# Kernel optimization log

Hardware: AMD Instinct MI355X
Metric: run time of the kernel (lower is better)

## Reference

```python
import jax, jax.numpy as jnp
import numpy as np


def setup_inputs() -> dict:
    key = jax.random.key(0)
    k1, k2, k3, k4 = jax.random.split(key, 4)
    B, C_in, C_out, E, K = 4, 128, 256, 30000, 5
    x = jax.random.normal(k1, (B, C_in, E, 1), dtype=jnp.float32)
    ne_idx = jax.random.randint(k2, (B, E, K - 1), 0, E, dtype=jnp.int32)
    conv_w = jax.random.normal(k3, (C_out, C_in, 1, K), dtype=jnp.float32) * 0.05
    conv_b = jax.random.normal(k4, (C_out,), dtype=jnp.float32) * 0.05
    return {"x": x, "ne_idx": ne_idx, "conv_w": conv_w, "conv_b": conv_b}


def reference(x, ne_idx, conv_w, conv_b):
    # x: [B, C, E, 1] edge features; ne_idx: [B, E, 4] neighbor edge ids.
    B, C, E, _ = x.shape
    xs = x[..., 0]                                        # [B, C, E]

    # pad_graph_mat: prepend self index column -> [B, E, 5]
    self_idx = jnp.broadcast_to(
        jnp.arange(E, dtype=ne_idx.dtype)[None, :, None], (B, E, 1))
    idx = jnp.concatenate([self_idx, ne_idx], axis=2) + 1  # +1 for zero pad slot

    # zero-pad feature dim so index 0 maps to zeros (matches torch padding col)
    x_pad = jnp.pad(xs, ((0, 0), (0, 0), (1, 0)))          # [B, C, E+1]

    # gather: f[b, c, e, k] = x_pad[b, c, idx[b, e, k]]
    f = jax.vmap(lambda xp, i: xp[:, i])(x_pad, idx)       # [B, C, E, 5]

    e0, e1, e2, e3, e4 = (f[..., j] for j in range(5))
    p = e1 + e3
    q = e2 + e4
    p1 = jnp.abs(e1 - e3)
    q1 = jnp.abs(e2 - e4)
    G = jnp.stack([e0, p, q, p1, q1], axis=-1)             # [B, C, E, 5]

    # Conv2d with kernel (1, 5): contraction over in-channels and the 5 taps
    out = jnp.einsum('bcek,ocuk->boe', G, conv_w) + conv_b[None, :, None]
    return out[..., None]                                  # [B, C_out, E, 1]
```

## Files before the change

### kernel.cpp

```cpp
#include <hip/hip_runtime.h>
#include <hip/hip_bf16.h>
#include <stdint.h>

#define E_N   30000
#define C_IN  128
#define C_OUT 256
#define B_N   4
#define KTAP  5
#define BN    64
#define KSTEPS 20

typedef short bf16x8 __attribute__((ext_vector_type(8)));
typedef float f32x4  __attribute__((ext_vector_type(4)));

static __device__ __forceinline__ unsigned short f2bf(float f) {
    union { float f; uint32_t u; } v; v.f = f;
    uint32_t r = (v.u + 0x7FFFu + ((v.u >> 16) & 1u)) >> 16;
    return (unsigned short)r;
}
static __device__ __forceinline__ float bf2f(uint32_t h) {
    union { uint32_t u; float f; } v; v.u = h << 16;
    return v.f;
}

__global__ void pack_w_kernel(const float* __restrict__ w,
                              unsigned short* __restrict__ wp) {
    int tid = blockIdx.x * blockDim.x + threadIdx.x;
    if (tid >= KSTEPS * 16 * 64) return;
    int s    = tid >> 10;
    int mt   = (tid >> 6) & 15;
    int lane = tid & 63;
    int m    = mt * 16 + (lane & 15);
    int kb   = s * 32 + ((lane >> 4) & 3) * 8;
    uint32_t pv[4];
    for (int jj = 0; jj < 4; ++jj) {
        unsigned short lo, hi;
        {
            int kk = kb + 2 * jj;
            int t = kk >> 7, c = kk & 127;
            lo = f2bf(w[(m * C_IN + c) * KTAP + t]);
        }
        {
            int kk = kb + 2 * jj + 1;
            int t = kk >> 7, c = kk & 127;
            hi = f2bf(w[(m * C_IN + c) * KTAP + t]);
        }
        pv[jj] = (uint32_t)lo | ((uint32_t)hi << 16);
    }
    uint4 val; val.x = pv[0]; val.y = pv[1]; val.z = pv[2]; val.w = pv[3];
    *(uint4*)(wp + (size_t)tid * 8) = val;
}

__global__ void transpose_kernel(const float* __restrict__ x,
                                 unsigned short* __restrict__ xT) {
    __shared__ float ld[C_IN][64 + 1];
    int b  = blockIdx.y;
    int e0 = blockIdx.x * 64;
    int t  = threadIdx.x;
    bool full = (e0 + 64 <= E_N);
    for (int pass = 0; pass < 8; ++pass) {
        int c  = pass * 16 + (t >> 4);
        int eo = (t & 15) * 4;
        if (full) {
            const float4 v = *(const float4*)(x + ((size_t)(b * C_IN + c) * E_N + e0 + eo));
            ld[c][eo] = v.x; ld[c][eo + 1] = v.y; ld[c][eo + 2] = v.z; ld[c][eo + 3] = v.w;
        } else {
            for (int i = 0; i < 4; ++i) {
                int e = e0 + eo + i;
                ld[c][eo + i] = (e < E_N) ? x[(size_t)(b * C_IN + c) * E_N + e] : 0.f;
            }
        }
    }
    __syncthreads();
    for (int pass = 0; pass < 8; ++pass) {
        int el = pass * 8 + (t >> 5);
        int c0 = (t & 31) * 4;
        int e  = e0 + el;
        if (e < E_N) {
            ushort4 v;
            v.x = f2bf(ld[c0 + 0][el]);
            v.y = f2bf(ld[c0 + 1][el]);
            v.z = f2bf(ld[c0 + 2][el]);
            v.w = f2bf(ld[c0 + 3][el]);
            *(ushort4*)(xT + (size_t)(b * E_N + e) * C_IN + c0) = v;
        }
    }
}

__launch_bounds__(256)
__global__ void mesh_gemm(const unsigned short* __restrict__ wp,
                          const unsigned short* __restrict__ xT,
                          const int* __restrict__ ne,
                          const float* __restrict__ bias,
                          float* __restrict__ out) {
    __shared__ __align__(16) unsigned short gbuf[BN][40];
    __shared__ int nbr[BN][4];

    int b    = blockIdx.y;
    int e0   = blockIdx.x * BN;
    int tid  = threadIdx.x;
    int lane = tid & 63;
    int wave = tid >> 6;

    {
        int col = tid >> 2, j = tid & 3;
        int e = e0 + col; if (e >= E_N) e = E_N - 1;
        nbr[col][j] = ne[((size_t)b * E_N + e) * 4 + j];
    }
    __syncthreads();

    f32x4 acc[4][4];
    for (int mt = 0; mt < 4; ++mt)
        for (int nt = 0; nt < 4; ++nt)
            acc[mt][nt] = (f32x4){0.f, 0.f, 0.f, 0.f};

    const int col    = tid >> 2;
    const int c8     = (tid & 3) * 8;
    int self_e       = e0 + col; if (self_e >= E_N) self_e = E_N - 1;
    const uint4* wp16 = (const uint4*)wp;

    for (int s = 0; s < KSTEPS; ++s) {
        const int tap = s >> 2;
        const int cb  = (s & 3) * 32;

        bf16x8 af[4];
        for (int mt = 0; mt < 4; ++mt) {
            int mtg = wave * 4 + mt;
            uint4 v = wp16[(s * 16 + mtg) * 64 + lane];
            af[mt] = *(bf16x8*)&v;
        }

        __syncthreads();

        {
            uint4 gval;
            if (tap == 0) {
                gval = *(const uint4*)(xT + ((size_t)(b * E_N + self_e) * C_IN + cb + c8));
            } else {
                int j1 = (tap == 1 || tap == 3) ? 0 : 1;
                int s1 = nbr[col][j1];
                int s2 = nbr[col][j1 + 2];
                uint4 v1 = *(const uint4*)(xT + ((size_t)(b * E_N + s1) * C_IN + cb + c8));
                uint4 v2 = *(const uint4*)(xT + ((size_t)(b * E_N + s2) * C_IN + cb + c8));
                const bool isabs = (tap >= 3);
                uint32_t* a1 = (uint32_t*)&v1;
                uint32_t* a2 = (uint32_t*)&v2;
                uint32_t* g  = (uint32_t*)&gval;
                for (int i = 0; i < 4; ++i) {
                    float x0 = bf2f(a1[i] & 0xFFFFu), x1 = bf2f(a1[i] >> 16);
                    float y0 = bf2f(a2[i] & 0xFFFFu), y1 = bf2f(a2[i] >> 16);
                    float r0 = isabs ? fabsf(x0 - y0) : (x0 + y0);
                    float r1 = isabs ? fabsf(x1 - y1) : (x1 + y1);
                    g[i] = (uint32_t)f2bf(r0) | ((uint32_t)f2bf(r1) << 16);
                }
            }
            *(uint4*)(&gbuf[col][c8]) = gval;
        }
        __syncthreads();

        bf16x8 bfr[4];
        const int nl_lo = lane & 15;
        const int k8    = ((lane >> 4) & 3) * 8;
        for (int nt = 0; nt < 4; ++nt)
            bfr[nt] = *(const bf16x8*)(&gbuf[nt * 16 + nl_lo][k8]);

        for (int nt = 0; nt < 4; ++nt)
            for (int mt = 0; mt < 4; ++mt)
                acc[mt][nt] = __builtin_amdgcn_mfma_f32_16x16x32_bf16(
                    af[mt], bfr[nt], acc[mt][nt], 0, 0, 0);
    }

    const int quad = lane >> 4;
    const int ecol = lane & 15;
    for (int mt = 0; mt < 4; ++mt) {
        int o_base = (wave * 4 + mt) * 16 + quad * 4;
        for (int r = 0; r < 4; ++r) {
            int o = o_base + r;
            float bv = bias[o];
            for (int nt = 0; nt < 4; ++nt) {
                int e = e0 + nt * 16 + ecol;
                if (e < E_N)
                    out[((size_t)(b * C_OUT + o)) * E_N + e] = acc[mt][nt][r] + bv;
            }
        }
    }
}

__global__ void fallback_kernel(const float* __restrict__ x,
                                const int* __restrict__ ne,
                                const float* __restrict__ w,
                                const float* __restrict__ bias,
                                float* __restrict__ out) {
    size_t id = (size_t)blockIdx.x * blockDim.x + threadIdx.x;
    if (id >= (size_t)B_N * C_OUT * E_N) return;
    int e = (int)(id % E_N);
    int o = (int)((id / E_N) % C_OUT);
    int b = (int)(id / ((size_t)E_N * C_OUT));
    const int4 nb = *(const int4*)(ne + ((size_t)b * E_N + e) * 4);
    float acc = bias[o];
    for (int c = 0; c < C_IN; ++c) {
        const float* xb = x + (size_t)(b * C_IN + c) * E_N;
        float s0 = xb[e];
        float x1 = xb[nb.x], x2 = xb[nb.y], x3 = xb[nb.z], x4 = xb[nb.w];
        const float* wo = w + (size_t)(o * C_IN + c) * KTAP;
        acc += wo[0] * s0
             + wo[1] * (x1 + x3)
             + wo[2] * (x2 + x4)
             + wo[3] * fabsf(x1 - x3)
             + wo[4] * fabsf(x2 - x4);
    }
    out[id] = acc;
}

extern "C" void kernel_launch(void* const* d_in, const int* in_sizes, int n_in,
                              void* d_out, int out_size, void* d_ws, size_t ws_size,
                              hipStream_t stream) {
    const float* x      = (const float*)d_in[0];
    const int*   ne_idx = (const int*)d_in[1];
    const float* conv_w = (const float*)d_in[2];
    const float* conv_b = (const float*)d_in[3];
    float* out = (float*)d_out;

    const size_t wp_bytes = (size_t)C_OUT * 640 * 2;
    const size_t xT_off   = 512 * 1024;
    const size_t need     = xT_off + (size_t)B_N * E_N * C_IN * 2;

    if (ws_size < need) {
        size_t total = (size_t)B_N * C_OUT * E_N;
        int blocks = (int)((total + 255) / 256);
        fallback_kernel<<<blocks, 256, 0, stream>>>(x, ne_idx, conv_w, conv_b, out);
        return;
    }
    (void)wp_bytes;

    unsigned short* wp = (unsigned short*)d_ws;
    unsigned short* xT = (unsigned short*)((char*)d_ws + xT_off);

    pack_w_kernel<<<80, 256, 0, stream>>>(conv_w, wp);
    dim3 tg((E_N + 63) / 64, B_N);
    transpose_kernel<<<tg, 256, 0, stream>>>(x, xT);
    dim3 gg((E_N + BN - 1) / BN, B_N);
    mesh_gemm<<<gg, 256, 0, stream>>>(wp, xT, ne_idx, conv_b, out);
}
```

Measured before the change: 256.3 us.

## Restructure mesh GEMM to gather all taps per channel chunk with prefetch

The main loop now runs over channel chunks instead of tap-major k-steps. For each chunk it loads the self and four neighbor rows once, computes all five tap features into a five-slot shared buffer, and prefetches the next chunk's rows while the MFMAs for the current chunk run. This cuts the number of barriers from 40 to 8 and removes redundant neighbor reloads. It also widens the transpose stores to 16 bytes and makes the output stores nontemporal. In exchange it uses more LDS and registers, which may lower occupancy.

```diff
diff --git a/kernel.cpp b/kernel.cpp
--- a/kernel.cpp
+++ b/kernel.cpp
@@ -8,7 +8,6 @@
 #define B_N   4
 #define KTAP  5
 #define BN    64
-#define KSTEPS 20
 
 typedef short bf16x8 __attribute__((ext_vector_type(8)));
 typedef float f32x4  __attribute__((ext_vector_type(4)));
@@ -26,7 +25,7 @@
 __global__ void pack_w_kernel(const float* __restrict__ w,
                               unsigned short* __restrict__ wp) {
     int tid = blockIdx.x * blockDim.x + threadIdx.x;
-    if (tid >= KSTEPS * 16 * 64) return;
+    if (tid >= 20 * 16 * 64) return;
     int s    = tid >> 10;
     int mt   = (tid >> 6) & 15;
     int lane = tid & 63;
@@ -72,17 +71,19 @@
         }
     }
     __syncthreads();
-    for (int pass = 0; pass < 8; ++pass) {
-        int el = pass * 8 + (t >> 5);
-        int c0 = (t & 31) * 4;
+    for (int pass = 0; pass < 4; ++pass) {
+        int el = pass * 16 + (t >> 4);
+        int c0 = (t & 15) * 8;
         int e  = e0 + el;
         if (e < E_N) {
-            ushort4 v;
-            v.x = f2bf(ld[c0 + 0][el]);
-            v.y = f2bf(ld[c0 + 1][el]);
-            v.z = f2bf(ld[c0 + 2][el]);
-            v.w = f2bf(ld[c0 + 3][el]);
-            *(ushort4*)(xT + (size_t)(b * E_N + e) * C_IN + c0) = v;
+            uint32_t pk[4];
+            for (int i = 0; i < 4; ++i) {
+                unsigned short lo = f2bf(ld[c0 + 2 * i][el]);
+                unsigned short hi = f2bf(ld[c0 + 2 * i + 1][el]);
+                pk[i] = (uint32_t)lo | ((uint32_t)hi << 16);
+            }
+            uint4 v; v.x = pk[0]; v.y = pk[1]; v.z = pk[2]; v.w = pk[3];
+            *(uint4*)(xT + (size_t)(b * E_N + e) * C_IN + c0) = v;
         }
     }
 }
@@ -93,14 +94,14 @@
                           const int* __restrict__ ne,
                           const float* __restrict__ bias,
                           float* __restrict__ out) {
-    __shared__ __align__(16) unsigned short gbuf[BN][40];
+    __shared__ __align__(16) unsigned short gbuf[KTAP][BN][40];
     __shared__ int nbr[BN][4];
 
-    int b    = blockIdx.y;
-    int e0   = blockIdx.x * BN;
-    int tid  = threadIdx.x;
-    int lane = tid & 63;
-    int wave = tid >> 6;
+    const int b    = blockIdx.y;
+    const int e0   = blockIdx.x * BN;
+    const int tid  = threadIdx.x;
+    const int lane = tid & 63;
+    const int wave = tid >> 6;
 
     {
         int col = tid >> 2, j = tid & 3;
@@ -109,78 +110,113 @@
     }
     __syncthreads();
 
+    const int col = tid >> 2;
+    const int c8  = (tid & 3) * 8;
+    int self_e = e0 + col; if (self_e >= E_N) self_e = E_N - 1;
+    const int s1 = nbr[col][0], s2 = nbr[col][2];
+    const int s3 = nbr[col][1], s4 = nbr[col][3];
+
+    const unsigned short* xb = xT + (size_t)b * E_N * C_IN + c8;
+    const uint4* p0 = (const uint4*)(xb + (size_t)self_e * C_IN);
+    const uint4* p1 = (const uint4*)(xb + (size_t)s1 * C_IN);
+    const uint4* p2 = (const uint4*)(xb + (size_t)s2 * C_IN);
+    const uint4* p3 = (const uint4*)(xb + (size_t)s3 * C_IN);
+    const uint4* p4 = (const uint4*)(xb + (size_t)s4 * C_IN);
+
     f32x4 acc[4][4];
+#pragma unroll
     for (int mt = 0; mt < 4; ++mt)
+#pragma unroll
         for (int nt = 0; nt < 4; ++nt)
             acc[mt][nt] = (f32x4){0.f, 0.f, 0.f, 0.f};
 
-    const int col    = tid >> 2;
-    const int c8     = (tid & 3) * 8;
-    int self_e       = e0 + col; if (self_e >= E_N) self_e = E_N - 1;
     const uint4* wp16 = (const uint4*)wp;
-
-    for (int s = 0; s < KSTEPS; ++s) {
-        const int tap = s >> 2;
-        const int cb  = (s & 3) * 32;
-
-        bf16x8 af[4];
-        for (int mt = 0; mt < 4; ++mt) {
-            int mtg = wave * 4 + mt;
-            uint4 v = wp16[(s * 16 + mtg) * 64 + lane];
-            af[mt] = *(bf16x8*)&v;
-        }
+    const int nl = lane & 15;
+    const int k8 = (lane >> 4) * 8;
+
+    uint4 v0 = p0[0], v1 = p1[0], v2 = p2[0], v3 = p3[0], v4 = p4[0];
+
+#pragma unroll
+    for (int cbi = 0; cbi < 4; ++cbi) {
+        uint4 g1, g2, g3, g4;
+        {
+            const uint32_t* a = (const uint32_t*)&v1;
+            const uint32_t* c = (const uint32_t*)&v2;
+            uint32_t* o1 = (uint32_t*)&g1;
+            uint32_t* o3 = (uint32_t*)&g3;
+#pragma unroll
+            for (int i = 0; i < 4; ++i) {
+                float x0 = bf2f(a[i] & 0xFFFFu), x1 = bf2f(a[i] >> 16);
+                float y0 = bf2f(c[i] & 0xFFFFu), y1 = bf2f(c[i] >> 16);
+                o1[i] = (uint32_t)f2bf(x0 + y0) | ((uint32_t)f2bf(x1 + y1) << 16);
+                o3[i] = (uint32_t)f2bf(fabsf(x0 - y0)) | ((uint32_t)f2bf(fabsf(x1 - y1)) << 16);
+            }
+            const uint32_t* d = (const uint32_t*)&v3;
+            const uint32_t* e = (const uint32_t*)&v4;
+            uint32_t* o2 = (uint32_t*)&g2;
+            uint32_t* o4 = (uint32_t*)&g4;
+#pragma unroll
+            for (int i = 0; i < 4; ++i) {
+                float x0 = bf2f(d[i] & 0xFFFFu), x1 = bf2f(d[i] >> 16);
+                float y0 = bf2f(e[i] & 0xFFFFu), y1 = bf2f(e[i] >> 16);
+                o2[i] = (uint32_t)f2bf(x0 + y0) | ((uint32_t)f2bf(x1 + y1) << 16);
+                o4[i] = (uint32_t)f2bf(fabsf(x0 - y0)) | ((uint32_t)f2bf(fabsf(x1 - y1)) << 16);
+            }
+        }
+        uint4 g0 = v0;
 
         __syncthreads();
-
-        {
-            uint4 gval;
-            if (tap == 0) {
-                gval = *(const uint4*)(xT + ((size_t)(b * E_N + self_e) * C_IN + cb + c8));
-            } else {
-                int j1 = (tap == 1 || tap == 3) ? 0 : 1;
-                int s1 = nbr[col][j1];
-                int s2 = nbr[col][j1 + 2];
-                uint4 v1 = *(const uint4*)(xT + ((size_t)(b * E_N + s1) * C_IN + cb + c8));
-                uint4 v2 = *(const uint4*)(xT + ((size_t)(b * E_N + s2) * C_IN + cb + c8));
-                const bool isabs = (tap >= 3);
-                uint32_t* a1 = (uint32_t*)&v1;
-                uint32_t* a2 = (uint32_t*)&v2;
-                uint32_t* g  = (uint32_t*)&gval;
-                for (int i = 0; i < 4; ++i) {
-                    float x0 = bf2f(a1[i] & 0xFFFFu), x1 = bf2f(a1[i] >> 16);
-                    float y0 = bf2f(a2[i] & 0xFFFFu), y1 = bf2f(a2[i] >> 16);
-                    float r0 = isabs ? fabsf(x0 - y0) : (x0 + y0);
-                    float r1 = isabs ? fabsf(x1 - y1) : (x1 + y1);
-                    g[i] = (uint32_t)f2bf(r0) | ((uint32_t)f2bf(r1) << 16);
-                }
-            }
-            *(uint4*)(&gbuf[col][c8]) = gval;
-        }
+        *(uint4*)(&gbuf[0][col][c8]) = g0;
+        *(uint4*)(&gbuf[1][col][c8]) = g1;
+        *(uint4*)(&gbuf[2][col][c8]) = g2;
+        *(uint4*)(&gbuf[3][col][c8]) = g3;
+        *(uint4*)(&gbuf[4][col][c8]) = g4;
         __syncthreads();
 
-        bf16x8 bfr[4];
-        const int nl_lo = lane & 15;
-        const int k8    = ((lane >> 4) & 3) * 8;
-        for (int nt = 0; nt < 4; ++nt)
-            bfr[nt] = *(const bf16x8*)(&gbuf[nt * 16 + nl_lo][k8]);
-
-        for (int nt = 0; nt < 4; ++nt)
-            for (int mt = 0; mt < 4; ++mt)
-                acc[mt][nt] = __builtin_amdgcn_mfma_f32_16x16x32_bf16(
-                    af[mt], bfr[nt], acc[mt][nt], 0, 0, 0);
+        if (cbi < 3) {
+            v0 = p0[4 * (cbi + 1)];
+            v1 = p1[4 * (cbi + 1)];
+            v2 = p2[4 * (cbi + 1)];
+            v3 = p3[4 * (cbi + 1)];
+            v4 = p4[4 * (cbi + 1)];
+        }
+
+#pragma unroll
+        for (int t = 0; t < KTAP; ++t) {
+            const int s = t * 4 + cbi;
+            bf16x8 af[4];
+#pragma unroll
+            for (int mt = 0; mt < 4; ++mt) {
+                uint4 w4 = wp16[(s * 16 + wave * 4 + mt) * 64 + lane];
+                af[mt] = *(bf16x8*)&w4;
+            }
+#pragma unroll
+            for (int nt = 0; nt < 4; ++nt) {
+                bf16x8 bf = *(const bf16x8*)(&gbuf[t][nt * 16 + nl][k8]);
+#pragma unroll
+                for (int mt = 0; mt < 4; ++mt)
+                    acc[mt][nt] = __builtin_amdgcn_mfma_f32_16x16x32_bf16(
+                        af[mt], bf, acc[mt][nt], 0, 0, 0);
+            }
+        }
     }
 
     const int quad = lane >> 4;
     const int ecol = lane & 15;
+#pragma unroll
     for (int mt = 0; mt < 4; ++mt) {
         int o_base = (wave * 4 + mt) * 16 + quad * 4;
+#pragma unroll
         for (int r = 0; r < 4; ++r) {
             int o = o_base + r;
             float bv = bias[o];
+#pragma unroll
             for (int nt = 0; nt < 4; ++nt) {
                 int e = e0 + nt * 16 + ecol;
                 if (e < E_N)
-                    out[((size_t)(b * C_OUT + o)) * E_N + e] = acc[mt][nt][r] + bv;
+                    __builtin_nontemporal_store(
+                        acc[mt][nt][r] + bv,
+                        &out[((size_t)(b * C_OUT + o)) * E_N + e]);
             }
         }
     }
@@ -221,9 +257,8 @@
     const float* conv_b = (const float*)d_in[3];
     float* out = (float*)d_out;
 
-    const size_t wp_bytes = (size_t)C_OUT * 640 * 2;
-    const size_t xT_off   = 512 * 1024;
-    const size_t need     = xT_off + (size_t)B_N * E_N * C_IN * 2;
+    const size_t xT_off = 512 * 1024;
+    const size_t need   = xT_off + (size_t)B_N * E_N * C_IN * 2;
 
     if (ws_size < need) {
         size_t total = (size_t)B_N * C_OUT * E_N;
@@ -231,7 +266,6 @@
         fallback_kernel<<<blocks, 256, 0, stream>>>(x, ne_idx, conv_w, conv_b, out);
         return;
     }
-    (void)wp_bytes;
 
     unsigned short* wp = (unsigned short*)d_ws;
     unsigned short* xT = (unsigned short*)((char*)d_ws + xT_off);
```

Result: slower. 262.0 us (+2.2%).
